# Optimization experiments

Hardware: AMD Instinct MI355X
Metric: run time of the kernel (lower is better)

Reference implementation:

```python
import jax, jax.numpy as jnp
import numpy as np

B, C, T, H, W = 8, 3, 16, 64, 64
CIN = C * T          # 48, conv in_channels
CQK = CIN // 8       # 6, query/key channels


def setup_inputs() -> dict:
    key = jax.random.key(0)
    ks = jax.random.split(key, 8)
    s = 0.05
    return {
        "x": jax.random.normal(ks[0], (B, C, T, H, W), dtype=jnp.float32),
        "Wq": jax.random.normal(ks[1], (CQK, CIN), dtype=jnp.float32) * s,
        "bq": jax.random.normal(ks[2], (CQK,), dtype=jnp.float32) * s,
        "Wk": jax.random.normal(ks[3], (CQK, CIN), dtype=jnp.float32) * s,
        "bk": jax.random.normal(ks[4], (CQK,), dtype=jnp.float32) * s,
        "Wv": jax.random.normal(ks[5], (CIN, CIN), dtype=jnp.float32) * s,
        "bv": jax.random.normal(ks[6], (CIN,), dtype=jnp.float32) * s,
        "gamma": jax.random.normal(ks[7], (1,), dtype=jnp.float32) * s,
    }


def reference(x, Wq, bq, Wk, bk, Wv, bv, gamma):
    b, c, t, h, w = x.shape
    n = h * w
    # merge channel and time dims: [B, C*T, H*W]
    x2 = x.reshape(b, c * t, n)
    # 1x1 convs are per-position channel matmuls
    q = jnp.einsum('oc,bcn->bon', Wq, x2) + bq[None, :, None]   # [B, CQK, N]
    k = jnp.einsum('oc,bcn->bon', Wk, x2) + bk[None, :, None]   # [B, CQK, N]
    v = jnp.einsum('oc,bcn->bon', Wv, x2) + bv[None, :, None]   # [B, CIN, N]
    # energy[b, i, j] = <q[:, i], k[:, j]>
    energy = jnp.einsum('bci,bcj->bij', q, k)                   # [B, N, N]
    attn = jax.nn.softmax(energy, axis=-1)
    # out[b, c, i] = sum_j v[b, c, j] * attn[b, i, j]
    out = jnp.einsum('bcj,bij->bci', v, attn)                   # [B, CIN, N]
    out = gamma[0] * out + x2
    return out.reshape(b, c, t, h, w)
```

## Files before the change

kernel.cpp:

```cpp
#include <hip/hip_runtime.h>

#define B_    8
#define CIN   48
#define CQK   6
#define N_    4096
#define CV    64
#define TI    64
#define TJ    64
#define NCH   4
#define JCH   (N_ / NCH)
#define TILES (JCH / TJ)

typedef __attribute__((ext_vector_type(8)))  short short8;
typedef __attribute__((ext_vector_type(16))) float f32x16;

__device__ __forceinline__ unsigned short f2bf(float f) {
    unsigned int u = __float_as_uint(f);
    u += 0x7FFFu + ((u >> 16) & 1u);
    return (unsigned short)(u >> 16);
}

__device__ __forceinline__ unsigned int cvt_pk_bf16(float a, float b) {
    unsigned int r;
    asm("v_cvt_pk_bf16_f32 %0, %1, %2" : "=v"(r) : "v"(a), "v"(b));
    return r;
}

__device__ __forceinline__ void pl32swap(unsigned int& x, unsigned int& y) {
    asm("v_permlane32_swap_b32 %0, %1" : "+v"(x), "+v"(y));
}

__device__ __forceinline__ short8 mk8(unsigned int w0, unsigned int w1,
                                      unsigned int w2, unsigned int w3) {
    union { unsigned int u[4]; short8 s; } t;
    t.u[0] = w0; t.u[1] = w1; t.u[2] = w2; t.u[3] = w3;
    return t.s;
}

__device__ __forceinline__ void cp16(const unsigned short* g, unsigned short* l) {
    __builtin_amdgcn_global_load_lds(
        (const __attribute__((address_space(1))) unsigned int*)g,
        (__attribute__((address_space(3))) unsigned int*)l, 16, 0, 0);
}

__global__ __launch_bounds__(256) void qkv_kernel(
    const float* __restrict__ x,
    const float* __restrict__ Wq, const float* __restrict__ bq,
    const float* __restrict__ Wk, const float* __restrict__ bk,
    const float* __restrict__ Wv, const float* __restrict__ bv,
    unsigned short* __restrict__ qB, unsigned short* __restrict__ kB,
    unsigned short* __restrict__ vB)
{
    __shared__ float sWq[CQK * CIN], sWk[CQK * CIN], sWv[CIN * CIN];
    __shared__ float sbq[CQK], sbk[CQK], sbv[CIN];
    const int tid = threadIdx.x;
    for (int idx = tid; idx < CQK * CIN; idx += 256) { sWq[idx] = Wq[idx]; sWk[idx] = Wk[idx]; }
    for (int idx = tid; idx < CIN * CIN; idx += 256) sWv[idx] = Wv[idx];
    if (tid < CQK) { sbq[tid] = bq[tid]; sbk[tid] = bk[tid]; }
    if (tid < CIN) sbv[tid] = bv[tid];
    __syncthreads();

    const int b   = blockIdx.x >> 7;
    const int sub = blockIdx.x & 127;
    const int pg  = sub >> 1;
    const int p   = sub & 1;
    const int g   = tid >> 6;
    const int n   = (pg << 6) + (tid & 63);

    float xc[CIN];
    const float* xb = x + ((size_t)b * CIN) * N_ + n;
#pragma unroll
    for (int c = 0; c < CIN; ++c) xc[c] = xb[(size_t)c * N_];

    if (p == 0) {
        if (g < 2) {
            const float* W  = g ? sWk : sWq;
            const float* bb = g ? sbk : sbq;
            short8 row = {0,0,0,0,0,0,0,0};
#pragma unroll
            for (int o = 0; o < CQK; ++o) {
                float s = bb[o];
#pragma unroll
                for (int c = 0; c < CIN; ++c) s += W[o * CIN + c] * xc[c];
                row[o] = (short)f2bf(s);
            }
            if (g == 0) {
                *(short8*)&qB[((size_t)b * N_ + n) * 8] = row;
                vB[((size_t)b * CV + 48) * N_ + n] = 0x3F80u;
#pragma unroll
                for (int o = 49; o < CV; ++o) vB[((size_t)b * CV + o) * N_ + n] = 0;
            } else {
                *(short8*)&kB[((size_t)b * N_ + n) * 8] = row;
            }
        } else {
            const int o0 = (g - 2) * 8;
#pragma unroll
            for (int oo = 0; oo < 8; ++oo) {
                const int o = o0 + oo;
                float sv = sbv[o];
#pragma unroll
                for (int c = 0; c < CIN; ++c) sv += sWv[o * CIN + c] * xc[c];
                vB[((size_t)b * CV + o) * N_ + n] = f2bf(sv);
            }
        }
    } else {
        const int o0 = 16 + g * 8;
#pragma unroll
        for (int oo = 0; oo < 8; ++oo) {
            const int o = o0 + oo;
            float sv = sbv[o];
#pragma unroll
            for (int c = 0; c < CIN; ++c) sv += sWv[o * CIN + c] * xc[c];
            vB[((size_t)b * CV + o) * N_ + n] = f2bf(sv);
        }
    }
}

__global__ __launch_bounds__(512, 4) void attn_kernel(
    const unsigned short* __restrict__ qB, const unsigned short* __restrict__ kB,
    const unsigned short* __restrict__ vB, const float* __restrict__ x,
    const float* __restrict__ gamma, float* __restrict__ out)
{
    __shared__ __align__(16) unsigned short vt[2][NCH][CV][TJ];
    float (*cbuf)[TI + 1] = (float (*)[TI + 1]) & vt[0][0][0][0];

    const int tid   = threadIdx.x;
    const int l     = tid & 63;
    const int w     = tid >> 6;
    const int chunk = w & 3;
    const int iw    = w >> 2;
    const int hi    = l >> 5;
    const int li    = l & 31;
    const int b     = blockIdx.x >> 6;
    const int ig    = blockIdx.x & 63;
    const int i_base = ig * TI;
    const int gx    = (l & 7) ^ ((l >> 3) & 7);

    const unsigned short* kg = kB + (size_t)b * N_ * 8;
    const unsigned short* vg = vB + (size_t)b * CV * N_;

    short8 qf = {0,0,0,0,0,0,0,0};
    if (hi == 0)
        qf = *(const short8*)&qB[((size_t)b * N_ + i_base + iw * 32 + li) * 8];

    f32x16 zc, acc0, acc1;
#pragma unroll
    for (int r = 0; r < 16; ++r) { zc[r] = 0.f; acc0[r] = 0.f; acc1[r] = 0.f; }

#define STAGE(BF, J0)                                                          \
    {                                                                          \
        _Pragma("unroll")                                                      \
        for (int s = 0; s < 4; ++s) {                                          \
            const int c = iw * 32 + s * 8 + (l >> 3);                          \
            cp16(&vg[(size_t)c * N_ + (J0) + gx * 8],                          \
                 &vt[BF][chunk][iw * 32 + s * 8][0]);                          \
        }                                                                      \
    }

#define DO_JST(JST, KF, VTC)                                                   \
    {                                                                          \
        f32x16 s = __builtin_amdgcn_mfma_f32_32x32x16_bf16(KF, qf, zc, 0, 0, 0);\
        _Pragma("unroll")                                                      \
        for (int r = 0; r < 16; ++r) s[r] = __expf(s[r]);                      \
        unsigned int c00 = cvt_pk_bf16(s[0],  s[1]);                           \
        unsigned int c10 = cvt_pk_bf16(s[2],  s[3]);                           \
        unsigned int c01 = cvt_pk_bf16(s[4],  s[5]);                           \
        unsigned int c11 = cvt_pk_bf16(s[6],  s[7]);                           \
        unsigned int c02 = cvt_pk_bf16(s[8],  s[9]);                           \
        unsigned int c12 = cvt_pk_bf16(s[10], s[11]);                          \
        unsigned int c03 = cvt_pk_bf16(s[12], s[13]);                          \
        unsigned int c13 = cvt_pk_bf16(s[14], s[15]);                          \
        unsigned int x0 = c00, y0 = c01; pl32swap(x0, y0);                     \
        unsigned int x1 = c10, y1 = c11; pl32swap(x1, y1);                     \
        const short8 pa0 = mk8(x0, x1, y0, y1);                                \
        unsigned int x2 = c02, y2 = c03; pl32swap(x2, y2);                     \
        unsigned int x3 = c12, y3 = c13; pl32swap(x3, y3);                     \
        const short8 pa1 = mk8(x2, x3, y2, y3);                                \
        const char* vrow0 = (const char*)&(VTC)[li][0];                        \
        const char* vrow1 = (const char*)&(VTC)[32 + li][0];                   \
        short8 vf;                                                             \
        vf = *(const short8*)(vrow0 + ((((JST)*4 + 0 + hi) ^ (li & 7)) << 4)); \
        acc0 = __builtin_amdgcn_mfma_f32_32x32x16_bf16(pa0, vf, acc0, 0, 0, 0);\
        vf = *(const short8*)(vrow0 + ((((JST)*4 + 2 + hi) ^ (li & 7)) << 4)); \
        acc0 = __builtin_amdgcn_mfma_f32_32x32x16_bf16(pa1, vf, acc0, 0, 0, 0);\
        vf = *(const short8*)(vrow1 + ((((JST)*4 + 0 + hi) ^ (li & 7)) << 4)); \
        acc1 = __builtin_amdgcn_mfma_f32_32x32x16_bf16(pa0, vf, acc1, 0, 0, 0);\
        vf = *(const short8*)(vrow1 + ((((JST)*4 + 2 + hi) ^ (li & 7)) << 4)); \
        acc1 = __builtin_amdgcn_mfma_f32_32x32x16_bf16(pa1, vf, acc1, 0, 0, 0);\
    }

    const int jbase = chunk * JCH;
    STAGE(0, jbase)
    short8 kf0  = {0,0,0,0,0,0,0,0}, kf1  = {0,0,0,0,0,0,0,0};
    short8 kf0n = {0,0,0,0,0,0,0,0}, kf1n = {0,0,0,0,0,0,0,0};
    if (hi == 0) {
        kf0 = *(const short8*)&kg[(size_t)(jbase + li) * 8];
        kf1 = *(const short8*)&kg[(size_t)(jbase + 32 + li) * 8];
    }
    asm volatile("s_waitcnt vmcnt(0)" ::: "memory");
    __syncthreads();

#pragma unroll 1
    for (int t = 0; t < TILES; ++t) {
        const int bf = t & 1;
        if (t + 1 < TILES) {
            const int j0n = jbase + (t + 1) * TJ;
            STAGE(bf ^ 1, j0n)
            if (hi == 0) {
                kf0n = *(const short8*)&kg[(size_t)(j0n + li) * 8];
                kf1n = *(const short8*)&kg[(size_t)(j0n + 32 + li) * 8];
            }
        }
        __builtin_amdgcn_s_setprio(1);
        DO_JST(0, kf0, vt[bf][chunk])
        DO_JST(1, kf1, vt[bf][chunk])
        __builtin_amdgcn_s_setprio(0);
        asm volatile("s_waitcnt vmcnt(0)" ::: "memory");
        __syncthreads();
        kf0 = kf0n; kf1 = kf1n;
    }
#undef DO_JST
#undef STAGE

#pragma unroll 1
    for (int r = 0; r < NCH; ++r) {
        if (chunk == r) {
#pragma unroll
            for (int reg = 0; reg < 16; ++reg) {
                const int i_loc = iw * 32 + (reg & 3) + 8 * (reg >> 2) + 4 * hi;
                if (r == 0) {
                    cbuf[li][i_loc]      = acc0[reg];
                    cbuf[32 + li][i_loc] = acc1[reg];
                } else {
                    cbuf[li][i_loc]      += acc0[reg];
                    cbuf[32 + li][i_loc] += acc1[reg];
                }
            }
        }
        __syncthreads();
    }

    const float gm = gamma[0];
#pragma unroll
    for (int rep = 0; rep < 8; ++rep) {
        const int idx = tid + rep * 512;
        const int c   = idx >> 6;
        const int i2  = idx & 63;
        if (c < CIN) {
            const size_t off = ((size_t)b * CIN + c) * N_ + i_base + i2;
            out[off] = gm * (cbuf[c][i2] / cbuf[48][i2]) + x[off];
        }
    }
}

extern "C" void kernel_launch(void* const* d_in, const int* in_sizes, int n_in,
                              void* d_out, int out_size, void* d_ws, size_t ws_size,
                              hipStream_t stream)
{
    const float* x     = (const float*)d_in[0];
    const float* Wq    = (const float*)d_in[1];
    const float* bq    = (const float*)d_in[2];
    const float* Wk    = (const float*)d_in[3];
    const float* bk    = (const float*)d_in[4];
    const float* Wv    = (const float*)d_in[5];
    const float* bv    = (const float*)d_in[6];
    const float* gamma = (const float*)d_in[7];
    float* out = (float*)d_out;

    unsigned short* qB = (unsigned short*)d_ws;
    unsigned short* kB = qB + (size_t)B_ * N_ * 8;
    unsigned short* vB = kB + (size_t)B_ * N_ * 8;

    qkv_kernel<<<dim3(B_ * 128), dim3(256), 0, stream>>>(
        x, Wq, bq, Wk, bk, Wv, bv, qB, kB, vB);
    attn_kernel<<<dim3(B_ * 64), dim3(512), 0, stream>>>(
        qB, kB, vB, x, gamma, out);
}
```

Baseline: 56.53 us.

## Fold log2e into keys, use raw exp2, restructure QKV split and loop barrier

Result: faster. 51.01 us (-9.8%).

```diff
diff --git a/kernel.cpp b/kernel.cpp
--- a/kernel.cpp
+++ b/kernel.cpp
@@ -10,6 +10,7 @@
 #define NCH   4
 #define JCH   (N_ / NCH)
 #define TILES (JCH / TJ)
+#define LOG2E 1.4426950408889634f
 
 typedef __attribute__((ext_vector_type(8)))  short short8;
 typedef __attribute__((ext_vector_type(16))) float f32x16;
@@ -18,6 +19,12 @@
     unsigned int u = __float_as_uint(f);
     u += 0x7FFFu + ((u >> 16) & 1u);
     return (unsigned short)(u >> 16);
+}
+
+__device__ __forceinline__ float exp2_fast(float x) {
+    float r;
+    asm("v_exp_f32 %0, %1" : "=v"(r) : "v"(x));
+    return r;
 }
 
 __device__ __forceinline__ unsigned int cvt_pk_bf16(float a, float b) {
@@ -60,54 +67,43 @@
     if (tid < CIN) sbv[tid] = bv[tid];
     __syncthreads();
 
-    const int b   = blockIdx.x >> 7;
-    const int sub = blockIdx.x & 127;
-    const int pg  = sub >> 1;
-    const int p   = sub & 1;
-    const int g   = tid >> 6;
-    const int n   = (pg << 6) + (tid & 63);
+    const int b = blockIdx.x >> 5;
+    const int n = ((blockIdx.x & 31) << 7) + (tid & 127);
+    const int h = tid >> 7;
 
     float xc[CIN];
     const float* xb = x + ((size_t)b * CIN) * N_ + n;
 #pragma unroll
     for (int c = 0; c < CIN; ++c) xc[c] = xb[(size_t)c * N_];
 
-    if (p == 0) {
-        if (g < 2) {
-            const float* W  = g ? sWk : sWq;
-            const float* bb = g ? sbk : sbq;
-            short8 row = {0,0,0,0,0,0,0,0};
-#pragma unroll
-            for (int o = 0; o < CQK; ++o) {
-                float s = bb[o];
-#pragma unroll
-                for (int c = 0; c < CIN; ++c) s += W[o * CIN + c] * xc[c];
-                row[o] = (short)f2bf(s);
+    if (h == 0) {
+        short8 qrow = {0,0,0,0,0,0,0,0}, krow = {0,0,0,0,0,0,0,0};
+#pragma unroll
+        for (int o = 0; o < CQK; ++o) {
+            float sq = sbq[o], sk = sbk[o];
+#pragma unroll
+            for (int c = 0; c < CIN; ++c) {
+                sq += sWq[o * CIN + c] * xc[c];
+                sk += sWk[o * CIN + c] * xc[c];
             }
-            if (g == 0) {
-                *(short8*)&qB[((size_t)b * N_ + n) * 8] = row;
-                vB[((size_t)b * CV + 48) * N_ + n] = 0x3F80u;
-#pragma unroll
-                for (int o = 49; o < CV; ++o) vB[((size_t)b * CV + o) * N_ + n] = 0;
-            } else {
-                *(short8*)&kB[((size_t)b * N_ + n) * 8] = row;
-            }
-        } else {
-            const int o0 = (g - 2) * 8;
-#pragma unroll
-            for (int oo = 0; oo < 8; ++oo) {
-                const int o = o0 + oo;
-                float sv = sbv[o];
-#pragma unroll
-                for (int c = 0; c < CIN; ++c) sv += sWv[o * CIN + c] * xc[c];
-                vB[((size_t)b * CV + o) * N_ + n] = f2bf(sv);
-            }
+            qrow[o] = (short)f2bf(sq);
+            krow[o] = (short)f2bf(sk * LOG2E);
+        }
+        *(short8*)&qB[((size_t)b * N_ + n) * 8] = qrow;
+        *(short8*)&kB[((size_t)b * N_ + n) * 8] = krow;
+        vB[((size_t)b * CV + 48) * N_ + n] = 0x3F80u;
+#pragma unroll
+        for (int o = 49; o < CV; ++o) vB[((size_t)b * CV + o) * N_ + n] = 0;
+#pragma unroll
+        for (int o = 0; o < 20; ++o) {
+            float sv = sbv[o];
+#pragma unroll
+            for (int c = 0; c < CIN; ++c) sv += sWv[o * CIN + c] * xc[c];
+            vB[((size_t)b * CV + o) * N_ + n] = f2bf(sv);
         }
     } else {
-        const int o0 = 16 + g * 8;
-#pragma unroll
-        for (int oo = 0; oo < 8; ++oo) {
-            const int o = o0 + oo;
+#pragma unroll
+        for (int o = 20; o < CIN; ++o) {
             float sv = sbv[o];
 #pragma unroll
             for (int c = 0; c < CIN; ++c) sv += sWv[o * CIN + c] * xc[c];
@@ -131,8 +127,8 @@
     const int iw    = w >> 2;
     const int hi    = l >> 5;
     const int li    = l & 31;
-    const int b     = blockIdx.x >> 6;
-    const int ig    = blockIdx.x & 63;
+    const int b     = blockIdx.x & 7;
+    const int ig    = blockIdx.x >> 3;
     const int i_base = ig * TI;
     const int gx    = (l & 7) ^ ((l >> 3) & 7);
 
@@ -161,7 +157,7 @@
     {                                                                          \
         f32x16 s = __builtin_amdgcn_mfma_f32_32x32x16_bf16(KF, qf, zc, 0, 0, 0);\
         _Pragma("unroll")                                                      \
-        for (int r = 0; r < 16; ++r) s[r] = __expf(s[r]);                      \
+        for (int r = 0; r < 16; ++r) s[r] = exp2_fast(s[r]);                   \
         unsigned int c00 = cvt_pk_bf16(s[0],  s[1]);                           \
         unsigned int c10 = cvt_pk_bf16(s[2],  s[3]);                           \
         unsigned int c01 = cvt_pk_bf16(s[4],  s[5]);                           \
@@ -190,19 +186,20 @@
     }
 
     const int jbase = chunk * JCH;
-    STAGE(0, jbase)
     short8 kf0  = {0,0,0,0,0,0,0,0}, kf1  = {0,0,0,0,0,0,0,0};
     short8 kf0n = {0,0,0,0,0,0,0,0}, kf1n = {0,0,0,0,0,0,0,0};
+    STAGE(0, jbase)
     if (hi == 0) {
         kf0 = *(const short8*)&kg[(size_t)(jbase + li) * 8];
         kf1 = *(const short8*)&kg[(size_t)(jbase + 32 + li) * 8];
     }
-    asm volatile("s_waitcnt vmcnt(0)" ::: "memory");
-    __syncthreads();
 
 #pragma unroll 1
     for (int t = 0; t < TILES; ++t) {
         const int bf = t & 1;
+        asm volatile("s_waitcnt vmcnt(0)" ::: "memory");
+        __builtin_amdgcn_s_barrier();
+        __builtin_amdgcn_sched_barrier(0);
         if (t + 1 < TILES) {
             const int j0n = jbase + (t + 1) * TJ;
             STAGE(bf ^ 1, j0n)
@@ -215,12 +212,12 @@
         DO_JST(0, kf0, vt[bf][chunk])
         DO_JST(1, kf1, vt[bf][chunk])
         __builtin_amdgcn_s_setprio(0);
-        asm volatile("s_waitcnt vmcnt(0)" ::: "memory");
-        __syncthreads();
         kf0 = kf0n; kf1 = kf1n;
     }
 #undef DO_JST
 #undef STAGE
+
+    __syncthreads();
 
 #pragma unroll 1
     for (int r = 0; r < NCH; ++r) {
@@ -271,7 +268,7 @@
     unsigned short* kB = qB + (size_t)B_ * N_ * 8;
     unsigned short* vB = kB + (size_t)B_ * N_ * 8;
 
-    qkv_kernel<<<dim3(B_ * 128), dim3(256), 0, stream>>>(
+    qkv_kernel<<<dim3(B_ * 32), dim3(256), 0, stream>>>(
         x, Wq, bq, Wk, bk, Wv, bv, qB, kB, vB);
     attn_kernel<<<dim3(B_ * 64), dim3(512), 0, stream>>>(
         qB, kB, vB, x, gamma, out);
```
